# Kernel optimization log

Hardware: AMD Instinct MI355X
Metric: run time of the kernel (lower is better)

The kernel has to match this reference:

```python
import jax, jax.numpy as jnp
import numpy as np

GAMMA = 1.0

def setup_inputs() -> dict:
    key = jax.random.key(0)
    kx, ky = jax.random.split(key)
    x = jax.random.normal(kx, (8192, 64), dtype=jnp.float32)
    y = jax.random.normal(ky, (8192, 64), dtype=jnp.float32)
    return {"x": x, "y": y}

def reference(x, y):
    # RBF kernel K[b,a] = exp(-gamma * ||x_b - y_a||^2)
    # broadcast intermediate of the naive formulation (same math).
    x_sq = jnp.sum(x * x, axis=-1)                    # (B,)
    y_sq = jnp.sum(y * y, axis=-1)                    # (A,)
    xy = jnp.einsum('bd,ad->ba', x, y)                # (B, A) GEMM
    dist_sq = x_sq[:, None] + y_sq[None, :] - 2.0 * xy
    dist_sq = jnp.maximum(dist_sq, 0.0)               # numeric floor
    return jnp.exp(-GAMMA * dist_sq)
```

## Files before the change

kernel.cpp:

```cpp
#include <hip/hip_runtime.h>

#define D    64
#define NROW 8192

typedef _Float16 f16x8 __attribute__((ext_vector_type(8)));
typedef float    f32x4 __attribute__((ext_vector_type(4)));

__global__ __launch_bounds__(256, 3) void rbf_fused(const float* __restrict__ x,
                                                    const float* __restrict__ y,
                                                    float* __restrict__ out) {
    __shared__ __align__(16) char smem[32768];
    __shared__ float Ysq0[128];
    __shared__ float Ysq1[128];
    char* const YH = smem;
    char* const YL = smem + 16384;

    const int t    = threadIdx.x;
    const int col0 = blockIdx.x * 128;
    const int row0 = blockIdx.y * 128;

    {
        const int r    = t & 127;
        const int half = t >> 7;
        const int swz  = (r & 7) << 4;
        const float* yp = y + (size_t)(col0 + r) * D + half * 32;
        float ssq = 0.f;
#pragma unroll
        for (int it = 0; it < 4; ++it) {
            float4 b0 = *reinterpret_cast<const float4*>(yp + it * 8);
            float4 b1 = *reinterpret_cast<const float4*>(yp + it * 8 + 4);
            float v[8] = {b0.x, b0.y, b0.z, b0.w, b1.x, b1.y, b1.z, b1.w};
            f16x8 h, l;
#pragma unroll
            for (int j = 0; j < 8; ++j) {
                _Float16 hh = (_Float16)v[j];
                h[j] = hh;
                l[j] = (_Float16)(v[j] - (float)hh);
                ssq  = fmaf(v[j], v[j], ssq);
            }
            const int off = r * 128 + ((half * 64 + it * 16) ^ swz);
            *reinterpret_cast<f16x8*>(YH + off) = h;
            *reinterpret_cast<f16x8*>(YL + off) = l;
        }
        if (half == 0) Ysq0[r] = ssq; else Ysq1[r] = ssq;
    }

    const int lane = t & 63;
    const int w    = t >> 6;
    const int l15  = lane & 15;
    const int lg   = lane >> 4;

    f16x8 xh[2][2], xl[2][2];
    float xsq[2];
#pragma unroll
    for (int i = 0; i < 2; ++i) {
        const float* xp = x + (size_t)(row0 + w * 32 + i * 16 + l15) * D + lg * 8;
        float s = 0.f;
#pragma unroll
        for (int kh = 0; kh < 2; ++kh) {
            float4 a0 = *reinterpret_cast<const float4*>(xp + kh * 32);
            float4 a1 = *reinterpret_cast<const float4*>(xp + kh * 32 + 4);
            float v[8] = {a0.x, a0.y, a0.z, a0.w, a1.x, a1.y, a1.z, a1.w};
#pragma unroll
            for (int j = 0; j < 8; ++j) {
                _Float16 hh = (_Float16)v[j];
                xh[i][kh][j] = hh;
                xl[i][kh][j] = (_Float16)(v[j] - (float)hh);
                s = fmaf(v[j], v[j], s);
            }
        }
        s += __shfl_xor(s, 16);
        s += __shfl_xor(s, 32);
        xsq[i] = s;
    }
    __syncthreads();

    f32x4 acc[2][8];
#pragma unroll
    for (int i = 0; i < 2; ++i)
#pragma unroll
        for (int nt = 0; nt < 8; ++nt) acc[i][nt] = (f32x4){0.f, 0.f, 0.f, 0.f};

    const int swzA = (l15 & 7) << 4;
#pragma unroll
    for (int kh = 0; kh < 2; ++kh) {
        const int dsw = (kh * 64 + lg * 16) ^ swzA;
#pragma unroll
        for (int nt = 0; nt < 8; ++nt) {
            const int aoff = (nt * 16 + l15) * 128 + dsw;
            f16x8 yh = *reinterpret_cast<const f16x8*>(YH + aoff);
            f16x8 yl = *reinterpret_cast<const f16x8*>(YL + aoff);
            acc[0][nt] = __builtin_amdgcn_mfma_f32_16x16x32_f16(yh, xh[0][kh], acc[0][nt], 0, 0, 0);
            acc[1][nt] = __builtin_amdgcn_mfma_f32_16x16x32_f16(yh, xh[1][kh], acc[1][nt], 0, 0, 0);
            acc[0][nt] = __builtin_amdgcn_mfma_f32_16x16x32_f16(yl, xh[0][kh], acc[0][nt], 0, 0, 0);
            acc[1][nt] = __builtin_amdgcn_mfma_f32_16x16x32_f16(yl, xh[1][kh], acc[1][nt], 0, 0, 0);
            acc[0][nt] = __builtin_amdgcn_mfma_f32_16x16x32_f16(yh, xl[0][kh], acc[0][nt], 0, 0, 0);
            acc[1][nt] = __builtin_amdgcn_mfma_f32_16x16x32_f16(yh, xl[1][kh], acc[1][nt], 0, 0, 0);
        }
    }

#pragma unroll
    for (int nt = 0; nt < 8; ++nt) {
        const int c = nt * 16 + lg * 4;
        float4 p0 = *reinterpret_cast<const float4*>(&Ysq0[c]);
        float4 p1 = *reinterpret_cast<const float4*>(&Ysq1[c]);
        float ys[4] = {p0.x + p1.x, p0.y + p1.y, p0.z + p1.z, p0.w + p1.w};
#pragma unroll
        for (int i = 0; i < 2; ++i) {
#pragma unroll
            for (int r = 0; r < 4; ++r) {
                float d2 = fmaxf(fmaf(-2.f, acc[i][nt][r], xsq[i] + ys[r]), 0.f);
                acc[i][nt][r] = __expf(-d2);
            }
        }
    }
    __syncthreads();

    char* const S = smem;
#pragma unroll
    for (int p = 0; p < 2; ++p) {
#pragma unroll
        for (int k = 0; k < 4; ++k) {
#pragma unroll
            for (int i = 0; i < 2; ++i) {
                const int row = w * 32 + i * 16 + l15;
                const int off = row * 256 + ((k * 64 + lg * 16) ^ ((row & 15) << 4));
                *reinterpret_cast<f32x4*>(S + off) = acc[i][p * 4 + k];
            }
        }
#pragma unroll
        for (int it = 0; it < 8; ++it) {
            const int rloc = w * 32 + it * 4 + (lane >> 4);
            const int off  = rloc * 256 + ((l15 * 16) ^ ((rloc & 15) << 4));
            f32x4 v = *reinterpret_cast<const f32x4*>(S + off);
            *reinterpret_cast<f32x4*>(out + (size_t)(row0 + rloc) * NROW
                                          + col0 + p * 64 + l15 * 4) = v;
        }
    }
}

extern "C" void kernel_launch(void* const* d_in, const int* in_sizes, int n_in,
                              void* d_out, int out_size, void* d_ws, size_t ws_size,
                              hipStream_t stream) {
    const float* x = (const float*)d_in[0];
    const float* y = (const float*)d_in[1];
    float* out = (float*)d_out;
    (void)d_ws; (void)ws_size;

    rbf_fused<<<dim3(NROW / 128, NROW / 128), 256, 0, stream>>>(x, y, out);
}
```

Before: 67.23 us.

## Precompute row norms in a separate kernel and retile into 64x256 strips

Adds a small pre-kernel that computes squared norms of the x and y rows into workspace, so the main kernel no longer recomputes them per tile. The main kernel now uses 512-thread blocks covering 64 rows by 256 columns. It stages both x and y as split-f16 hi/lo in LDS, swizzles the block index to group neighbouring tiles, and writes full 1 KB output rows through an LDS transpose. This targets the store-bound output path and redundant norm work, at the cost of a second launch, 80 KB of LDS per block and lower occupancy.

```diff
diff --git a/kernel.cpp b/kernel.cpp
--- a/kernel.cpp
+++ b/kernel.cpp
@@ -6,27 +6,50 @@
 typedef _Float16 f16x8 __attribute__((ext_vector_type(8)));
 typedef float    f32x4 __attribute__((ext_vector_type(4)));
 
-__global__ __launch_bounds__(256, 3) void rbf_fused(const float* __restrict__ x,
+__global__ __launch_bounds__(256) void rbf_rowsq(const float* __restrict__ x,
+                                                 const float* __restrict__ y,
+                                                 float* __restrict__ sq) {
+    int tid = blockIdx.x * blockDim.x + threadIdx.x;
+    const float* src = (tid < NROW) ? x : y;
+    int row = tid & (NROW - 1);
+    const float4* p = reinterpret_cast<const float4*>(src + row * D);
+    float s = 0.f;
+#pragma unroll
+    for (int i = 0; i < D / 4; ++i) {
+        float4 v = p[i];
+        s = fmaf(v.x, v.x, s);
+        s = fmaf(v.y, v.y, s);
+        s = fmaf(v.z, v.z, s);
+        s = fmaf(v.w, v.w, s);
+    }
+    sq[tid] = s;
+}
+
+__global__ __launch_bounds__(512, 2) void rbf_strip(const float* __restrict__ x,
                                                     const float* __restrict__ y,
+                                                    const float* __restrict__ sq,
                                                     float* __restrict__ out) {
-    __shared__ __align__(16) char smem[32768];
-    __shared__ float Ysq0[128];
-    __shared__ float Ysq1[128];
+    __shared__ __align__(16) char smem[81920];
     char* const YH = smem;
-    char* const YL = smem + 16384;
+    char* const YL = smem + 32768;
+    char* const XH = smem + 65536;
+    char* const XL = smem + 73728;
+    char* const S  = smem;
 
-    const int t    = threadIdx.x;
-    const int col0 = blockIdx.x * 128;
-    const int row0 = blockIdx.y * 128;
+    const int t = threadIdx.x;
+
+    const int nb      = (blockIdx.x & 7) * 512 + (blockIdx.x >> 3);
+    const int row0    = (nb >> 5) * 64;
+    const int col0    = (nb & 31) * 256;
 
     {
-        const int r    = t & 127;
-        const int half = t >> 7;
+        const int r    = t & 255;
+        const int half = t >> 8;
         const int swz  = (r & 7) << 4;
         const float* yp = y + (size_t)(col0 + r) * D + half * 32;
-        float ssq = 0.f;
 #pragma unroll
         for (int it = 0; it < 4; ++it) {
+            const int c16 = half * 4 + it;
             float4 b0 = *reinterpret_cast<const float4*>(yp + it * 8);
             float4 b1 = *reinterpret_cast<const float4*>(yp + it * 8 + 4);
             float v[8] = {b0.x, b0.y, b0.z, b0.w, b1.x, b1.y, b1.z, b1.w};
@@ -36,106 +59,104 @@
                 _Float16 hh = (_Float16)v[j];
                 h[j] = hh;
                 l[j] = (_Float16)(v[j] - (float)hh);
-                ssq  = fmaf(v[j], v[j], ssq);
             }
-            const int off = r * 128 + ((half * 64 + it * 16) ^ swz);
+            const int off = r * 128 + ((c16 * 16) ^ swz);
             *reinterpret_cast<f16x8*>(YH + off) = h;
             *reinterpret_cast<f16x8*>(YL + off) = l;
         }
-        if (half == 0) Ysq0[r] = ssq; else Ysq1[r] = ssq;
     }
+    {
+        const int r   = t >> 3;
+        const int c16 = t & 7;
+        const int swz = (r & 7) << 4;
+        const float* xp = x + (size_t)(row0 + r) * D + c16 * 8;
+        float4 a0 = *reinterpret_cast<const float4*>(xp);
+        float4 a1 = *reinterpret_cast<const float4*>(xp + 4);
+        float v[8] = {a0.x, a0.y, a0.z, a0.w, a1.x, a1.y, a1.z, a1.w};
+        f16x8 h, l;
+#pragma unroll
+        for (int j = 0; j < 8; ++j) {
+            _Float16 hh = (_Float16)v[j];
+            h[j] = hh;
+            l[j] = (_Float16)(v[j] - (float)hh);
+        }
+        const int off = r * 128 + ((c16 * 16) ^ swz);
+        *reinterpret_cast<f16x8*>(XH + off) = h;
+        *reinterpret_cast<f16x8*>(XL + off) = l;
+    }
+    __syncthreads();
 
     const int lane = t & 63;
     const int w    = t >> 6;
     const int l15  = lane & 15;
     const int lg   = lane >> 4;
+    const int swzA = (l15 & 7) << 4;
 
-    f16x8 xh[2][2], xl[2][2];
-    float xsq[2];
+    f32x4 acc[2][4];
 #pragma unroll
-    for (int i = 0; i < 2; ++i) {
-        const float* xp = x + (size_t)(row0 + w * 32 + i * 16 + l15) * D + lg * 8;
-        float s = 0.f;
+    for (int mt = 0; mt < 2; ++mt)
 #pragma unroll
-        for (int kh = 0; kh < 2; ++kh) {
-            float4 a0 = *reinterpret_cast<const float4*>(xp + kh * 32);
-            float4 a1 = *reinterpret_cast<const float4*>(xp + kh * 32 + 4);
-            float v[8] = {a0.x, a0.y, a0.z, a0.w, a1.x, a1.y, a1.z, a1.w};
+        for (int nt = 0; nt < 4; ++nt) acc[mt][nt] = (f32x4){0.f, 0.f, 0.f, 0.f};
+
 #pragma unroll
-            for (int j = 0; j < 8; ++j) {
-                _Float16 hh = (_Float16)v[j];
-                xh[i][kh][j] = hh;
-                xl[i][kh][j] = (_Float16)(v[j] - (float)hh);
-                s = fmaf(v[j], v[j], s);
+    for (int kh = 0; kh < 2; ++kh) {
+        const int dsw = (kh * 64 + lg * 16) ^ swzA;
+        f16x8 yh[2], yl[2], bh[4], bl[4];
+#pragma unroll
+        for (int mt = 0; mt < 2; ++mt) {
+            const int aoff = (w * 32 + mt * 16 + l15) * 128 + dsw;
+            yh[mt] = *reinterpret_cast<const f16x8*>(YH + aoff);
+            yl[mt] = *reinterpret_cast<const f16x8*>(YL + aoff);
+        }
+#pragma unroll
+        for (int nt = 0; nt < 4; ++nt) {
+            const int boff = (nt * 16 + l15) * 128 + dsw;
+            bh[nt] = *reinterpret_cast<const f16x8*>(XH + boff);
+            bl[nt] = *reinterpret_cast<const f16x8*>(XL + boff);
+        }
+#pragma unroll
+        for (int mt = 0; mt < 2; ++mt)
+#pragma unroll
+            for (int nt = 0; nt < 4; ++nt) {
+                acc[mt][nt] = __builtin_amdgcn_mfma_f32_16x16x32_f16(yh[mt], bh[nt], acc[mt][nt], 0, 0, 0);
+                acc[mt][nt] = __builtin_amdgcn_mfma_f32_16x16x32_f16(yl[mt], bh[nt], acc[mt][nt], 0, 0, 0);
+                acc[mt][nt] = __builtin_amdgcn_mfma_f32_16x16x32_f16(yh[mt], bl[nt], acc[mt][nt], 0, 0, 0);
             }
-        }
-        s += __shfl_xor(s, 16);
-        s += __shfl_xor(s, 32);
-        xsq[i] = s;
+    }
+
+    float xsqv[4];
+#pragma unroll
+    for (int nt = 0; nt < 4; ++nt) xsqv[nt] = sq[row0 + nt * 16 + l15];
+#pragma unroll
+    for (int mt = 0; mt < 2; ++mt) {
+        float4 q = *reinterpret_cast<const float4*>(sq + NROW + col0 + w * 32 + mt * 16 + lg * 4);
+        float ys[4] = {q.x, q.y, q.z, q.w};
+#pragma unroll
+        for (int nt = 0; nt < 4; ++nt)
+#pragma unroll
+            for (int r = 0; r < 4; ++r) {
+                float d2 = fmaxf(fmaf(-2.f, acc[mt][nt][r], xsqv[nt] + ys[r]), 0.f);
+                acc[mt][nt][r] = __expf(-d2);
+            }
     }
     __syncthreads();
 
-    f32x4 acc[2][8];
 #pragma unroll
-    for (int i = 0; i < 2; ++i)
+    for (int mt = 0; mt < 2; ++mt)
 #pragma unroll
-        for (int nt = 0; nt < 8; ++nt) acc[i][nt] = (f32x4){0.f, 0.f, 0.f, 0.f};
-
-    const int swzA = (l15 & 7) << 4;
-#pragma unroll
-    for (int kh = 0; kh < 2; ++kh) {
-        const int dsw = (kh * 64 + lg * 16) ^ swzA;
-#pragma unroll
-        for (int nt = 0; nt < 8; ++nt) {
-            const int aoff = (nt * 16 + l15) * 128 + dsw;
-            f16x8 yh = *reinterpret_cast<const f16x8*>(YH + aoff);
-            f16x8 yl = *reinterpret_cast<const f16x8*>(YL + aoff);
-            acc[0][nt] = __builtin_amdgcn_mfma_f32_16x16x32_f16(yh, xh[0][kh], acc[0][nt], 0, 0, 0);
-            acc[1][nt] = __builtin_amdgcn_mfma_f32_16x16x32_f16(yh, xh[1][kh], acc[1][nt], 0, 0, 0);
-            acc[0][nt] = __builtin_amdgcn_mfma_f32_16x16x32_f16(yl, xh[0][kh], acc[0][nt], 0, 0, 0);
-            acc[1][nt] = __builtin_amdgcn_mfma_f32_16x16x32_f16(yl, xh[1][kh], acc[1][nt], 0, 0, 0);
-            acc[0][nt] = __builtin_amdgcn_mfma_f32_16x16x32_f16(yh, xl[0][kh], acc[0][nt], 0, 0, 0);
-            acc[1][nt] = __builtin_amdgcn_mfma_f32_16x16x32_f16(yh, xl[1][kh], acc[1][nt], 0, 0, 0);
+        for (int nt = 0; nt < 4; ++nt) {
+            const int srow = nt * 16 + l15;
+            const int off  = srow * 1024 + (((w * 8 + mt * 4 + lg) * 16) ^ ((srow & 7) << 4));
+            *reinterpret_cast<f32x4*>(S + off) = acc[mt][nt];
         }
-    }
+    __syncthreads();
 
 #pragma unroll
-    for (int nt = 0; nt < 8; ++nt) {
-        const int c = nt * 16 + lg * 4;
-        float4 p0 = *reinterpret_cast<const float4*>(&Ysq0[c]);
-        float4 p1 = *reinterpret_cast<const float4*>(&Ysq1[c]);
-        float ys[4] = {p0.x + p1.x, p0.y + p1.y, p0.z + p1.z, p0.w + p1.w};
-#pragma unroll
-        for (int i = 0; i < 2; ++i) {
-#pragma unroll
-            for (int r = 0; r < 4; ++r) {
-                float d2 = fmaxf(fmaf(-2.f, acc[i][nt][r], xsq[i] + ys[r]), 0.f);
-                acc[i][nt][r] = __expf(-d2);
-            }
-        }
-    }
-    __syncthreads();
-
-    char* const S = smem;
-#pragma unroll
-    for (int p = 0; p < 2; ++p) {
-#pragma unroll
-        for (int k = 0; k < 4; ++k) {
-#pragma unroll
-            for (int i = 0; i < 2; ++i) {
-                const int row = w * 32 + i * 16 + l15;
-                const int off = row * 256 + ((k * 64 + lg * 16) ^ ((row & 15) << 4));
-                *reinterpret_cast<f32x4*>(S + off) = acc[i][p * 4 + k];
-            }
-        }
-#pragma unroll
-        for (int it = 0; it < 8; ++it) {
-            const int rloc = w * 32 + it * 4 + (lane >> 4);
-            const int off  = rloc * 256 + ((l15 * 16) ^ ((rloc & 15) << 4));
-            f32x4 v = *reinterpret_cast<const f32x4*>(S + off);
-            *reinterpret_cast<f32x4*>(out + (size_t)(row0 + rloc) * NROW
-                                          + col0 + p * 64 + l15 * 4) = v;
-        }
+    for (int it = 0; it < 8; ++it) {
+        const int row = w * 8 + it;
+        const int off = row * 1024 + ((lane * 16) ^ ((row & 7) << 4));
+        f32x4 v = *reinterpret_cast<const f32x4*>(S + off);
+        *reinterpret_cast<f32x4*>(out + (size_t)(row0 + row) * NROW + col0 + lane * 4) = v;
     }
 }
 
@@ -145,7 +166,8 @@
     const float* x = (const float*)d_in[0];
     const float* y = (const float*)d_in[1];
     float* out = (float*)d_out;
-    (void)d_ws; (void)ws_size;
+    float* sq  = (float*)d_ws;
 
-    rbf_fused<<<dim3(NROW / 128, NROW / 128), 256, 0, stream>>>(x, y, out);
+    rbf_rowsq<<<64, 256, 0, stream>>>(x, y, sq);
+    rbf_strip<<<4096, 512, 0, stream>>>(x, y, sq, out);
 }
```

After: 73.82 us. +9.8%, slower.
